# Performance work log

Hardware: AMD Instinct MI355X
Metric: run time of the kernel (lower is better)

The kernel has to match this reference:

```python
import itertools
import jax, jax.numpy as jnp
import numpy as np

N1 = 4
N2 = 4
D = 3
BATCH = 512
NDENSE = 256
FEAT_IN = (N1 + N2) * D  # 24


def _perms_and_signs(n):
    P = np.array(list(itertools.permutations(range(n))), dtype=np.int32)  # [n!, n], lexicographic
    # sign = (-1)^(number of inversions)
    triu = np.triu(np.ones((n, n), dtype=np.int64), 1)
    inv = np.sum((P[:, :, None] > P[:, None, :]) * triu, axis=(1, 2))
    signs = np.where(inv % 2 == 0, 1.0, -1.0).astype(np.float32)
    return P, signs

P1_np, S1_np = _perms_and_signs(N1)
P2_np, S2_np = _perms_and_signs(N2)


def setup_inputs() -> dict:
    key = jax.random.key(0)
    ks = jax.random.split(key, 12)
    def dense_init(k, fan_in, fan_out):
        return jax.random.normal(k, (fan_in, fan_out), jnp.float32) / jnp.sqrt(jnp.float32(fan_in))
    inp = {
        "x1": jax.random.normal(ks[0], (BATCH, N1, D), jnp.float32),
        "x2": jax.random.normal(ks[1], (BATCH, N2, D), jnp.float32),
        "W0": dense_init(ks[2], FEAT_IN, NDENSE),
        "b0": jnp.zeros((NDENSE,), jnp.float32),
        "W1": dense_init(ks[3], NDENSE, NDENSE),
        "b1": jnp.zeros((NDENSE,), jnp.float32),
        "W2": dense_init(ks[4], NDENSE, NDENSE),
        "b2": jnp.zeros((NDENSE,), jnp.float32),
        "Wf": dense_init(ks[5], NDENSE, 1),
        "bf": jnp.zeros((1,), jnp.float32),
    }
    return inp


def _resnet(h, W0, b0, W1, b1, W2, b2, Wf, bf):
    # SimpleResNet: residual tanh dense layers (skip when shapes match), linear head
    y = jnp.tanh(h @ W0 + b0)            # [.., 24] -> [.., 256]: no skip (shape mismatch)
    y = jnp.tanh(y @ W1 + b1) + y        # residual
    y = jnp.tanh(y @ W2 + b2) + y        # residual
    return y @ Wf + bf                   # [.., 1], no activation


def reference(x1, x2, W0, b0, W1, b1, W2, b2, Wf, bf):
    P1 = jnp.asarray(P1_np); P2 = jnp.asarray(P2_np)
    s1 = jnp.asarray(S1_np); s2 = jnp.asarray(S2_np)
    nf1, nf2 = P1.shape[0], P2.shape[0]  # 24, 24
    # all permutations along particle axis
    p1 = jnp.take(x1, P1, axis=-2)       # [B, nf1, n1, d]
    p2 = jnp.take(x2, P2, axis=-2)       # [B, nf2, n2, d]
    # broadcast to cross product of permutation axes
    b1_ = jnp.broadcast_to(p1[:, :, None, :, :], (x1.shape[0], nf1, nf2, N1, D))
    b2_ = jnp.broadcast_to(p2[:, None, :, :, :], (x2.shape[0], nf1, nf2, N2, D))
    concat = jnp.concatenate([b1_, b2_], axis=-2)                  # [B, nf1, nf2, n1+n2, d]
    feats = concat.reshape(concat.shape[:-2] + (-1,))              # [B, nf1, nf2, (n1+n2)*d]
    out = _resnet(feats, W0, b0, W1, b1, W2, b2, Wf, bf)           # [B, nf1, nf2, 1]
    signed = out * s1[:, None, None] * s2[:, None]                 # sign-weighted
    anti = jnp.sum(signed, axis=(-1, -2, -3))                      # [B]
    return jnp.log(jnp.abs(anti))
```

## Files before the change

### kernel.cpp

```cpp
#include <hip/hip_runtime.h>
#include <math.h>

#define NPERM 24
#define ND 256
#define RPB 48
#define RPW 12
#define ROWS_PER_B 576
#define BATCH 512
#define TOTAL_ROWS (BATCH * ROWS_PER_B)
#define NBLOCKS (TOTAL_ROWS / RPB)

__constant__ int c_P[NPERM * 4] = {
    0,1,2,3, 0,1,3,2, 0,2,1,3, 0,2,3,1, 0,3,1,2, 0,3,2,1,
    1,0,2,3, 1,0,3,2, 1,2,0,3, 1,2,3,0, 1,3,0,2, 1,3,2,0,
    2,0,1,3, 2,0,3,1, 2,1,0,3, 2,1,3,0, 2,3,0,1, 2,3,1,0,
    3,0,1,2, 3,0,2,1, 3,1,0,2, 3,1,2,0, 3,2,0,1, 3,2,1,0
};
__constant__ float c_S[NPERM] = {
     1.f,-1.f,-1.f, 1.f, 1.f,-1.f,
    -1.f, 1.f, 1.f,-1.f,-1.f, 1.f,
     1.f,-1.f,-1.f, 1.f, 1.f,-1.f,
    -1.f, 1.f, 1.f,-1.f,-1.f, 1.f
};

__global__ __launch_bounds__(256, 2)
void fused_resnet(const float* __restrict__ x1, const float* __restrict__ x2,
                  const float* __restrict__ W0, const float* __restrict__ b0,
                  const float* __restrict__ W1, const float* __restrict__ b1,
                  const float* __restrict__ W2, const float* __restrict__ b2,
                  const float* __restrict__ Wf, const float* __restrict__ bf,
                  double* __restrict__ anti)
{
    __shared__ float sY[RPB * ND];
    __shared__ float sStage[4096];
    const int t   = threadIdx.x;
    const int tc  = t & 63;
    const int tr  = t >> 6;
    const int gr0 = blockIdx.x * RPB;
    const int b   = gr0 / ROWS_PER_B;

    for (int e = t; e < RPB * 24; e += 256) {
        int lr = e / 24, c = e % 24;
        int pp = (gr0 + lr) % ROWS_PER_B;
        float v;
        if (c < 12) {
            int p1 = pp / 24;
            v = x1[b * 12 + c_P[p1 * 4 + c / 3] * 3 + (c % 3)];
        } else {
            int p2 = pp % 24; int cc = c - 12;
            v = x2[b * 12 + c_P[p2 * 4 + cc / 3] * 3 + (cc % 3)];
        }
        sStage[2048 + e] = v;
    }

    float acc[RPW][4];

    #pragma unroll
    for (int r = 0; r < RPW; ++r) { acc[r][0]=0.f; acc[r][1]=0.f; acc[r][2]=0.f; acc[r][3]=0.f; }
    for (int kt = 0; kt < 24; kt += 8) {
        __syncthreads();
        {
            const float4* src = (const float4*)(W0 + kt * ND);
            float4* dst = (float4*)sStage;
            for (int i = t; i < (8 * ND) / 4; i += 256) dst[i] = src[i];
        }
        __syncthreads();
        #pragma unroll
        for (int k4 = 0; k4 < 2; ++k4) {
            float w[4][4];
            #pragma unroll
            for (int k = 0; k < 4; ++k) {
                float4 wv = *(const float4*)&sStage[(k4 * 4 + k) * ND + 4 * tc];
                w[k][0]=wv.x; w[k][1]=wv.y; w[k][2]=wv.z; w[k][3]=wv.w;
            }
            #pragma unroll
            for (int r = 0; r < RPW; ++r) {
                float4 yv = *(const float4*)&sStage[2048 + (tr * RPW + r) * 24 + kt + k4 * 4];
                float yk[4] = {yv.x, yv.y, yv.z, yv.w};
                #pragma unroll
                for (int k = 0; k < 4; ++k)
                    #pragma unroll
                    for (int c = 0; c < 4; ++c)
                        acc[r][c] = fmaf(yk[k], w[k][c], acc[r][c]);
            }
        }
    }
    {
        float4 bv = *(const float4*)&b0[4 * tc];
        float bb[4] = {bv.x, bv.y, bv.z, bv.w};
        __syncthreads();
        #pragma unroll
        for (int r = 0; r < RPW; ++r) {
            float4 o;
            o.x = tanhf(acc[r][0] + bb[0]);
            o.y = tanhf(acc[r][1] + bb[1]);
            o.z = tanhf(acc[r][2] + bb[2]);
            o.w = tanhf(acc[r][3] + bb[3]);
            *(float4*)&sY[(tr * RPW + r) * ND + 4 * tc] = o;
        }
        __syncthreads();
    }

    #pragma unroll 1
    for (int layer = 0; layer < 2; ++layer) {
        const float* W   = layer ? W2 : W1;
        const float* bbp = layer ? b2 : b1;
        #pragma unroll
        for (int r = 0; r < RPW; ++r) { acc[r][0]=0.f; acc[r][1]=0.f; acc[r][2]=0.f; acc[r][3]=0.f; }
        for (int kt = 0; kt < ND; kt += 16) {
            __syncthreads();
            {
                const float4* src = (const float4*)(W + kt * ND);
                float4* dst = (float4*)sStage;
                #pragma unroll
                for (int i = 0; i < 4; ++i) dst[t + i * 256] = src[t + i * 256];
            }
            __syncthreads();
            #pragma unroll
            for (int k4 = 0; k4 < 4; ++k4) {
                float w[4][4];
                #pragma unroll
                for (int k = 0; k < 4; ++k) {
                    float4 wv = *(const float4*)&sStage[(k4 * 4 + k) * ND + 4 * tc];
                    w[k][0]=wv.x; w[k][1]=wv.y; w[k][2]=wv.z; w[k][3]=wv.w;
                }
                #pragma unroll
                for (int r = 0; r < RPW; ++r) {
                    float4 yv = *(const float4*)&sY[(tr * RPW + r) * ND + kt + k4 * 4];
                    float yk[4] = {yv.x, yv.y, yv.z, yv.w};
                    #pragma unroll
                    for (int k = 0; k < 4; ++k)
                        #pragma unroll
                        for (int c = 0; c < 4; ++c)
                            acc[r][c] = fmaf(yk[k], w[k][c], acc[r][c]);
                }
            }
        }
        float4 bv = *(const float4*)&bbp[4 * tc];
        float bb[4] = {bv.x, bv.y, bv.z, bv.w};
        float ny[RPW][4];
        #pragma unroll
        for (int r = 0; r < RPW; ++r) {
            float4 yo = *(const float4*)&sY[(tr * RPW + r) * ND + 4 * tc];
            float yov[4] = {yo.x, yo.y, yo.z, yo.w};
            #pragma unroll
            for (int c = 0; c < 4; ++c)
                ny[r][c] = tanhf(acc[r][c] + bb[c]) + yov[c];
        }
        __syncthreads();
        #pragma unroll
        for (int r = 0; r < RPW; ++r) {
            float4 o; o.x = ny[r][0]; o.y = ny[r][1]; o.z = ny[r][2]; o.w = ny[r][3];
            *(float4*)&sY[(tr * RPW + r) * ND + 4 * tc] = o;
        }
        __syncthreads();
    }

    if (t < 64) {
        ((float4*)sStage)[t] = ((const float4*)Wf)[t];
    }
    __syncthreads();
    double contrib = 0.0;
    if (tc < RPW) {
        int row = tr * RPW + tc;
        const float* yrow = &sY[row * ND];
        float f = 0.f;
        #pragma unroll 8
        for (int k = 0; k < ND; ++k) f = fmaf(yrow[k], sStage[k], f);
        f += bf[0];
        int pp = (gr0 + row) % ROWS_PER_B;
        double s = (double)(c_S[pp / 24] * c_S[pp % 24]);
        contrib = s * (double)f;
    }
    #pragma unroll
    for (int off = 32; off > 0; off >>= 1) contrib += __shfl_xor(contrib, off, 64);
    if (tc == 0) atomicAdd(&anti[b], contrib);
}

__global__ void finalize_log(const double* __restrict__ anti, float* __restrict__ out) {
    int i = blockIdx.x * 256 + threadIdx.x;
    if (i < BATCH) out[i] = (float)log(fabs(anti[i]));
}

extern "C" void kernel_launch(void* const* d_in, const int* in_sizes, int n_in,
                              void* d_out, int out_size, void* d_ws, size_t ws_size,
                              hipStream_t stream) {
    const float* x1 = (const float*)d_in[0];
    const float* x2 = (const float*)d_in[1];
    const float* W0 = (const float*)d_in[2];
    const float* b0 = (const float*)d_in[3];
    const float* W1 = (const float*)d_in[4];
    const float* b1 = (const float*)d_in[5];
    const float* W2 = (const float*)d_in[6];
    const float* b2 = (const float*)d_in[7];
    const float* Wf = (const float*)d_in[8];
    const float* bf = (const float*)d_in[9];
    double* anti = (double*)d_ws;
    float* out   = (float*)d_out;

    hipMemsetAsync(anti, 0, BATCH * sizeof(double), stream);
    fused_resnet<<<NBLOCKS, 256, 0, stream>>>(x1, x2, W0, b0, W1, b1, W2, b2, Wf, bf, anti);
    finalize_log<<<(BATCH + 255) / 256, 256, 0, stream>>>(anti, out);
}
```

Baseline: 1.299 ms.

## Keep activations in registers, broadcast via readlane, shrink LDS for higher occupancy

Hidden activations now stay in per-thread registers instead of a 48x256 LDS buffer. Each layer's K operand is broadcast across the wavefront with readlane, which removes the LDS activation buffer and cuts shared memory to about 50KB. Launch bounds are raised to 3 blocks per CU, weight tiles grow to 32 rows with register double-buffering, and W0 and Wf are loaded once up front. The risks are serialized scalar readlane traffic (48 per k4 step) and register pressure at the higher occupancy target.

Result: slower. 1.916 ms (+47.5%).

```diff
diff --git a/kernel.cpp b/kernel.cpp
--- a/kernel.cpp
+++ b/kernel.cpp
@@ -1,29 +1,31 @@
 #include <hip/hip_runtime.h>
 #include <math.h>
 
-#define NPERM 24
 #define ND 256
 #define RPB 48
 #define RPW 12
 #define ROWS_PER_B 576
 #define BATCH 512
-#define TOTAL_ROWS (BATCH * ROWS_PER_B)
-#define NBLOCKS (TOTAL_ROWS / RPB)
-
-__constant__ int c_P[NPERM * 4] = {
+#define NBLOCKS (BATCH * ROWS_PER_B / RPB)
+
+__constant__ int c_P[24 * 4] = {
     0,1,2,3, 0,1,3,2, 0,2,1,3, 0,2,3,1, 0,3,1,2, 0,3,2,1,
     1,0,2,3, 1,0,3,2, 1,2,0,3, 1,2,3,0, 1,3,0,2, 1,3,2,0,
     2,0,1,3, 2,0,3,1, 2,1,0,3, 2,1,3,0, 2,3,0,1, 2,3,1,0,
     3,0,1,2, 3,0,2,1, 3,1,0,2, 3,1,2,0, 3,2,0,1, 3,2,1,0
 };
-__constant__ float c_S[NPERM] = {
+__constant__ float c_S[24] = {
      1.f,-1.f,-1.f, 1.f, 1.f,-1.f,
     -1.f, 1.f, 1.f,-1.f,-1.f, 1.f,
      1.f,-1.f,-1.f, 1.f, 1.f,-1.f,
     -1.f, 1.f, 1.f,-1.f,-1.f, 1.f
 };
 
-__global__ __launch_bounds__(256, 2)
+__device__ __forceinline__ float bcast(float v, int srcLane) {
+    return __int_as_float(__builtin_amdgcn_readlane(__float_as_int(v), srcLane));
+}
+
+__global__ __launch_bounds__(256, 3)
 void fused_resnet(const float* __restrict__ x1, const float* __restrict__ x2,
                   const float* __restrict__ W0, const float* __restrict__ b0,
                   const float* __restrict__ W1, const float* __restrict__ b1,
@@ -31,150 +33,154 @@
                   const float* __restrict__ Wf, const float* __restrict__ bf,
                   double* __restrict__ anti)
 {
-    __shared__ float sY[RPB * ND];
-    __shared__ float sStage[4096];
-    const int t   = threadIdx.x;
-    const int tc  = t & 63;
-    const int tr  = t >> 6;
-    const int gr0 = blockIdx.x * RPB;
-    const int b   = gr0 / ROWS_PER_B;
-
-    for (int e = t; e < RPB * 24; e += 256) {
-        int lr = e / 24, c = e % 24;
+    __shared__ __align__(16) float smem[12592];
+    float* sW  = smem;
+    float* sF  = smem + 8192;
+    float* sWf = smem + 12336;
+
+    const int t    = threadIdx.x;
+    const int lane = t & 63;
+    const int wv   = t >> 6;
+    const int r0   = wv * RPW;
+    const int gr0  = blockIdx.x * RPB;
+    const int b    = gr0 / ROWS_PER_B;
+
+    for (int i = t; i < RPB * 24; i += 256) {
+        int lr = i / 24, c = i % 24;
         int pp = (gr0 + lr) % ROWS_PER_B;
         float v;
         if (c < 12) {
-            int p1 = pp / 24;
-            v = x1[b * 12 + c_P[p1 * 4 + c / 3] * 3 + (c % 3)];
+            v = x1[b * 12 + c_P[(pp / 24) * 4 + c / 3] * 3 + (c % 3)];
         } else {
-            int p2 = pp % 24; int cc = c - 12;
-            v = x2[b * 12 + c_P[p2 * 4 + cc / 3] * 3 + (cc % 3)];
-        }
-        sStage[2048 + e] = v;
-    }
+            int cc = c - 12;
+            v = x2[b * 12 + c_P[(pp % 24) * 4 + cc / 3] * 3 + (cc % 3)];
+        }
+        sF[i] = v;
+    }
+    {
+        const float4* src = (const float4*)W0;
+        float4* dst = (float4*)sW;
+        #pragma unroll
+        for (int i = 0; i < 6; ++i) dst[t + 256 * i] = src[t + 256 * i];
+    }
+    if (t < 64) ((float4*)sWf)[t] = ((const float4*)Wf)[t];
+    __syncthreads();
 
     float acc[RPW][4];
+    float y[RPW][4];
 
     #pragma unroll
     for (int r = 0; r < RPW; ++r) { acc[r][0]=0.f; acc[r][1]=0.f; acc[r][2]=0.f; acc[r][3]=0.f; }
-    for (int kt = 0; kt < 24; kt += 8) {
-        __syncthreads();
-        {
-            const float4* src = (const float4*)(W0 + kt * ND);
-            float4* dst = (float4*)sStage;
-            for (int i = t; i < (8 * ND) / 4; i += 256) dst[i] = src[i];
-        }
-        __syncthreads();
-        #pragma unroll
-        for (int k4 = 0; k4 < 2; ++k4) {
-            float w[4][4];
+    #pragma unroll
+    for (int k4 = 0; k4 < 6; ++k4) {
+        float4 w[4];
+        #pragma unroll
+        for (int kk = 0; kk < 4; ++kk)
+            w[kk] = *(const float4*)&sW[(k4 * 4 + kk) * ND + 4 * lane];
+        #pragma unroll
+        for (int r = 0; r < RPW; ++r) {
+            float4 yv = *(const float4*)&sF[(r0 + r) * 24 + k4 * 4];
+            float yk[4] = {yv.x, yv.y, yv.z, yv.w};
             #pragma unroll
-            for (int k = 0; k < 4; ++k) {
-                float4 wv = *(const float4*)&sStage[(k4 * 4 + k) * ND + 4 * tc];
-                w[k][0]=wv.x; w[k][1]=wv.y; w[k][2]=wv.z; w[k][3]=wv.w;
+            for (int kk = 0; kk < 4; ++kk) {
+                acc[r][0] = fmaf(yk[kk], w[kk].x, acc[r][0]);
+                acc[r][1] = fmaf(yk[kk], w[kk].y, acc[r][1]);
+                acc[r][2] = fmaf(yk[kk], w[kk].z, acc[r][2]);
+                acc[r][3] = fmaf(yk[kk], w[kk].w, acc[r][3]);
             }
-            #pragma unroll
-            for (int r = 0; r < RPW; ++r) {
-                float4 yv = *(const float4*)&sStage[2048 + (tr * RPW + r) * 24 + kt + k4 * 4];
-                float yk[4] = {yv.x, yv.y, yv.z, yv.w};
-                #pragma unroll
-                for (int k = 0; k < 4; ++k)
-                    #pragma unroll
-                    for (int c = 0; c < 4; ++c)
-                        acc[r][c] = fmaf(yk[k], w[k][c], acc[r][c]);
-            }
         }
     }
     {
-        float4 bv = *(const float4*)&b0[4 * tc];
-        float bb[4] = {bv.x, bv.y, bv.z, bv.w};
-        __syncthreads();
+        float4 bv = *(const float4*)&b0[4 * lane];
         #pragma unroll
         for (int r = 0; r < RPW; ++r) {
-            float4 o;
-            o.x = tanhf(acc[r][0] + bb[0]);
-            o.y = tanhf(acc[r][1] + bb[1]);
-            o.z = tanhf(acc[r][2] + bb[2]);
-            o.w = tanhf(acc[r][3] + bb[3]);
-            *(float4*)&sY[(tr * RPW + r) * ND + 4 * tc] = o;
-        }
-        __syncthreads();
+            y[r][0] = tanhf(acc[r][0] + bv.x);
+            y[r][1] = tanhf(acc[r][1] + bv.y);
+            y[r][2] = tanhf(acc[r][2] + bv.z);
+            y[r][3] = tanhf(acc[r][3] + bv.w);
+        }
     }
 
     #pragma unroll 1
-    for (int layer = 0; layer < 2; ++layer) {
-        const float* W   = layer ? W2 : W1;
-        const float* bbp = layer ? b2 : b1;
+    for (int L = 0; L < 2; ++L) {
+        const float* __restrict__ Wg = L ? W2 : W1;
+        const float* __restrict__ bp = L ? b2 : b1;
         #pragma unroll
         for (int r = 0; r < RPW; ++r) { acc[r][0]=0.f; acc[r][1]=0.f; acc[r][2]=0.f; acc[r][3]=0.f; }
-        for (int kt = 0; kt < ND; kt += 16) {
+        #pragma unroll 1
+        for (int T = 0; T < 8; ++T) {
             __syncthreads();
             {
-                const float4* src = (const float4*)(W + kt * ND);
-                float4* dst = (float4*)sStage;
+                const float4* src = (const float4*)(Wg + T * 32 * ND);
+                float4* dst = (float4*)sW;
                 #pragma unroll
-                for (int i = 0; i < 4; ++i) dst[t + i * 256] = src[t + i * 256];
+                for (int i = 0; i < 8; ++i) dst[t + 256 * i] = src[t + 256 * i];
             }
             __syncthreads();
+            float4 wc[4], wn[4];
             #pragma unroll
-            for (int k4 = 0; k4 < 4; ++k4) {
-                float w[4][4];
+            for (int kk = 0; kk < 4; ++kk)
+                wc[kk] = *(const float4*)&sW[kk * ND + 4 * lane];
+            #pragma unroll 1
+            for (int k4 = 0; k4 < 8; ++k4) {
+                if (k4 < 7) {
+                    #pragma unroll
+                    for (int kk = 0; kk < 4; ++kk)
+                        wn[kk] = *(const float4*)&sW[((k4 + 1) * 4 + kk) * ND + 4 * lane];
+                }
+                const int sl = T * 8 + k4;
                 #pragma unroll
-                for (int k = 0; k < 4; ++k) {
-                    float4 wv = *(const float4*)&sStage[(k4 * 4 + k) * ND + 4 * tc];
-                    w[k][0]=wv.x; w[k][1]=wv.y; w[k][2]=wv.z; w[k][3]=wv.w;
+                for (int r = 0; r < RPW; ++r) {
+                    float ys[4];
+                    #pragma unroll
+                    for (int kk = 0; kk < 4; ++kk) ys[kk] = bcast(y[r][kk], sl);
+                    #pragma unroll
+                    for (int kk = 0; kk < 4; ++kk) {
+                        acc[r][0] = fmaf(ys[kk], wc[kk].x, acc[r][0]);
+                        acc[r][1] = fmaf(ys[kk], wc[kk].y, acc[r][1]);
+                        acc[r][2] = fmaf(ys[kk], wc[kk].z, acc[r][2]);
+                        acc[r][3] = fmaf(ys[kk], wc[kk].w, acc[r][3]);
+                    }
                 }
                 #pragma unroll
-                for (int r = 0; r < RPW; ++r) {
-                    float4 yv = *(const float4*)&sY[(tr * RPW + r) * ND + kt + k4 * 4];
-                    float yk[4] = {yv.x, yv.y, yv.z, yv.w};
-                    #pragma unroll
-                    for (int k = 0; k < 4; ++k)
-                        #pragma unroll
-                        for (int c = 0; c < 4; ++c)
-                            acc[r][c] = fmaf(yk[k], w[k][c], acc[r][c]);
-                }
+                for (int kk = 0; kk < 4; ++kk) wc[kk] = wn[kk];
             }
         }
-        float4 bv = *(const float4*)&bbp[4 * tc];
-        float bb[4] = {bv.x, bv.y, bv.z, bv.w};
-        float ny[RPW][4];
+        float4 bv = *(const float4*)&bp[4 * lane];
         #pragma unroll
         for (int r = 0; r < RPW; ++r) {
-            float4 yo = *(const float4*)&sY[(tr * RPW + r) * ND + 4 * tc];
-            float yov[4] = {yo.x, yo.y, yo.z, yo.w};
-            #pragma unroll
-            for (int c = 0; c < 4; ++c)
-                ny[r][c] = tanhf(acc[r][c] + bb[c]) + yov[c];
-        }
-        __syncthreads();
-        #pragma unroll
-        for (int r = 0; r < RPW; ++r) {
-            float4 o; o.x = ny[r][0]; o.y = ny[r][1]; o.z = ny[r][2]; o.w = ny[r][3];
-            *(float4*)&sY[(tr * RPW + r) * ND + 4 * tc] = o;
-        }
-        __syncthreads();
-    }
-
-    if (t < 64) {
-        ((float4*)sStage)[t] = ((const float4*)Wf)[t];
+            y[r][0] = tanhf(acc[r][0] + bv.x) + y[r][0];
+            y[r][1] = tanhf(acc[r][1] + bv.y) + y[r][1];
+            y[r][2] = tanhf(acc[r][2] + bv.z) + y[r][2];
+            y[r][3] = tanhf(acc[r][3] + bv.w) + y[r][3];
+        }
+    }
+
+    __syncthreads();
+    #pragma unroll
+    for (int r = 0; r < RPW; ++r) {
+        int row = r0 + r;
+        smem[row * 257 + 4 * lane + 0] = y[r][0];
+        smem[row * 257 + 4 * lane + 1] = y[r][1];
+        smem[row * 257 + 4 * lane + 2] = y[r][2];
+        smem[row * 257 + 4 * lane + 3] = y[r][3];
     }
     __syncthreads();
     double contrib = 0.0;
-    if (tc < RPW) {
-        int row = tr * RPW + tc;
-        const float* yrow = &sY[row * ND];
+    if (t < RPB) {
+        const float* yrow = &smem[t * 257];
         float f = 0.f;
         #pragma unroll 8
-        for (int k = 0; k < ND; ++k) f = fmaf(yrow[k], sStage[k], f);
+        for (int k = 0; k < ND; ++k) f = fmaf(yrow[k], sWf[k], f);
         f += bf[0];
-        int pp = (gr0 + row) % ROWS_PER_B;
-        double s = (double)(c_S[pp / 24] * c_S[pp % 24]);
-        contrib = s * (double)f;
-    }
-    #pragma unroll
-    for (int off = 32; off > 0; off >>= 1) contrib += __shfl_xor(contrib, off, 64);
-    if (tc == 0) atomicAdd(&anti[b], contrib);
+        int pp = (gr0 + t) % ROWS_PER_B;
+        contrib = (double)(c_S[pp / 24] * c_S[pp % 24]) * (double)f;
+    }
+    if (wv == 0) {
+        #pragma unroll
+        for (int off = 32; off > 0; off >>= 1) contrib += __shfl_xor(contrib, off, 64);
+        if (lane == 0) atomicAdd(&anti[b], contrib);
+    }
 }
 
 __global__ void finalize_log(const double* __restrict__ anti, float* __restrict__ out) {
@@ -198,7 +204,7 @@
     double* anti = (double*)d_ws;
     float* out   = (float*)d_out;
 
-    hipMemsetAsync(anti, 0, BATCH * sizeof(double), stream);
+    (void)hipMemsetAsync(anti, 0, BATCH * sizeof(double), stream);
     fused_resnet<<<NBLOCKS, 256, 0, stream>>>(x1, x2, W0, b0, W1, b1, W2, b2, Wf, bf, anti);
     finalize_log<<<(BATCH + 255) / 256, 256, 0, stream>>>(anti, out);
 }
```
